# Kernel optimization log

Measured on AMD Instinct MI355X. Metric: run time of the kernel, lower is better.

## Reference

```python
import jax, jax.numpy as jnp
import numpy as np

N, E, D, H, C, L = 100000, 1280000, 64, 4, 16, 3  # nodes, edges, dim, heads, head_dim, layers
NEG_SLOPE = 0.2
LN_EPS = 1e-5


def setup_inputs() -> dict:
    key = jax.random.key(0)
    ks = jax.random.split(key, 6)
    scale = 1.0 / np.sqrt(D)
    x = jax.random.normal(ks[0], (N, D), dtype=jnp.float32)
    edge_index = jax.random.randint(ks[1], (2, E), 0, N, dtype=jnp.int64)
    Wl = jax.random.normal(ks[2], (L, D, H * C), dtype=jnp.float32) * scale  # lin_l (source)
    Wr = jax.random.normal(ks[3], (L, D, H * C), dtype=jnp.float32) * scale  # lin_r (target)
    att = jax.random.normal(ks[4], (L, H, C), dtype=jnp.float32) * scale
    bias = jnp.zeros((L, H * C), dtype=jnp.float32)
    gamma = jnp.ones((L, D), dtype=jnp.float32)
    beta = jnp.zeros((L, D), dtype=jnp.float32)
    return dict(x=x, edge_index=edge_index, Wl=Wl, Wr=Wr, att=att, bias=bias, gamma=gamma, beta=beta)


def _gatv2_conv(x, src, dst, Wl, Wr, att, bias):
    # GATv2Conv (concat=True, share_weights=False, negative_slope=0.2)
    n = x.shape[0]
    xl = (x @ Wl).reshape(n, H, C)  # messages from source nodes
    xr = (x @ Wr).reshape(n, H, C)  # target-side transform
    m = xl[src] + xr[dst]  # [E', H, C]
    e = jnp.einsum('ehc,hc->eh', jax.nn.leaky_relu(m, NEG_SLOPE), att)  # [E', H]
    emax = jax.ops.segment_max(e, dst, num_segments=n)
    p = jnp.exp(e - emax[dst])
    denom = jax.ops.segment_sum(p, dst, num_segments=n)
    alpha = p / denom[dst]  # self-loops guarantee denom > 0
    out = jax.ops.segment_sum(alpha[:, :, None] * xl[src], dst, num_segments=n)  # [N, H, C]
    return out.reshape(n, H * C) + bias


def _layernorm(x, gamma, beta):
    mu = jnp.mean(x, axis=-1, keepdims=True)
    var = jnp.mean(jnp.square(x - mu), axis=-1, keepdims=True)
    return (x - mu) * jax.lax.rsqrt(var + LN_EPS) * gamma + beta


def reference(x, edge_index, Wl, Wr, att, bias, gamma, beta):
    n = x.shape[0]
    loops = jnp.arange(n, dtype=edge_index.dtype)
    src = jnp.concatenate([edge_index[0], loops])  # PyG add_self_loops=True
    dst = jnp.concatenate([edge_index[1], loops])
    for i in range(L):
        x_res = x
        x = _gatv2_conv(x, src, dst, Wl[i], Wr[i], att[i], bias[i])
        x = x + x_res  # residual
        x = _layernorm(x, gamma[i], beta[i])
        x = jax.nn.gelu(x, approximate=False)
    return x
```

## Files before the change

kernel.cpp:

```cpp
#include <hip/hip_runtime.h>
#include <math.h>


#define SCAN_CHUNK 1024

typedef __attribute__((ext_vector_type(8))) short short8;
typedef __attribute__((ext_vector_type(4))) float f32x4;

static inline int cdiv(int a, int b) { return (a + b - 1) / b; }

__device__ __forceinline__ unsigned short bf16_rtn(float v) {
    unsigned u = __float_as_uint(v);
    return (unsigned short)((u + 0x7fffu + ((u >> 16) & 1u)) >> 16);
}


__global__ void detect_i64(const unsigned int* __restrict__ ei, int* __restrict__ flag) {
    if (threadIdx.x == 0 && blockIdx.x == 0) {
        int is64 = 1;
        #pragma unroll 1
        for (int i = 0; i < 64; ++i)
            if (ei[2 * i + 1] != 0u) { is64 = 0; break; }
        *flag = is64;
    }
}

__global__ void init_deg(int* __restrict__ deg, int N) {
    int i = blockIdx.x * blockDim.x + threadIdx.x;
    if (i < N) deg[i] = 1;
}

__global__ void hist_kernel(const int* __restrict__ ei, int E, const int* __restrict__ flag,
                            int* __restrict__ deg, int* __restrict__ pos) {
    int e = blockIdx.x * blockDim.x + threadIdx.x;
    if (e >= E) return;
    int is64 = *flag;
    int d = is64 ? ei[2 * (E + e)] : ei[E + e];
    pos[e] = atomicAdd(&deg[d], 1);
}

__global__ void scan_blocks(const int* __restrict__ deg, int* __restrict__ rowptr,
                            int* __restrict__ partials, int N) {
    __shared__ int sdata[256];
    int t = threadIdx.x;
    int idx0 = blockIdx.x * SCAN_CHUNK + t * 4;
    int v[4]; int sum = 0;
    #pragma unroll
    for (int i = 0; i < 4; ++i) {
        int ii = idx0 + i;
        v[i] = (ii < N) ? deg[ii] : 0;
        sum += v[i];
    }
    sdata[t] = sum;
    __syncthreads();
    for (int off = 1; off < 256; off <<= 1) {
        int val = 0;
        if (t >= off) val = sdata[t - off];
        __syncthreads();
        if (t >= off) sdata[t] += val;
        __syncthreads();
    }
    int run = (t > 0) ? sdata[t - 1] : 0;
    #pragma unroll
    for (int i = 0; i < 4; ++i) {
        int ii = idx0 + i;
        if (ii < N) rowptr[ii] = run;
        run += v[i];
    }
    if (t == 255) partials[blockIdx.x] = sdata[255];
}

__global__ void scan_partials_k(int* __restrict__ partials, int NB) {
    __shared__ int sd[256];
    int t = threadIdx.x;
    sd[t] = (t < NB) ? partials[t] : 0;
    __syncthreads();
    for (int off = 1; off < 256; off <<= 1) {
        int val = 0;
        if (t >= off) val = sd[t - off];
        __syncthreads();
        if (t >= off) sd[t] += val;
        __syncthreads();
    }
    if (t < NB) partials[t] = (t > 0) ? sd[t - 1] : 0;
}

__global__ void add_offsets(int* __restrict__ rowptr, const int* __restrict__ partials,
                            int N, int Etot) {
    int i = blockIdx.x * blockDim.x + threadIdx.x;
    if (i < N) rowptr[i] += partials[i / SCAN_CHUNK];
    if (i == 0) rowptr[N] = Etot;
}

__global__ void fill_csr(const int* __restrict__ ei, int E, int N, const int* __restrict__ flag,
                         const int* __restrict__ rowptr, const int* __restrict__ pos,
                         int* __restrict__ col) {
    int i = blockIdx.x * blockDim.x + threadIdx.x;
    if (i >= E + N) return;
    if (i < E) {
        int is64 = *flag;
        int s = is64 ? ei[2 * i] : ei[i];
        int d = is64 ? ei[2 * (E + i)] : ei[E + i];
        col[rowptr[d] + pos[i]] = s;
    } else {
        int nn = i - E;
        col[rowptr[nn]] = nn;
    }
}


__global__ __launch_bounds__(256) void cast_hi_lo(
    const float* __restrict__ x, unsigned short* __restrict__ hi,
    unsigned short* __restrict__ lo, int total4) {
    int i = blockIdx.x * blockDim.x + threadIdx.x;
    int stride = gridDim.x * blockDim.x;
    for (; i < total4; i += stride) {
        float4 v = ((const float4*)x)[i];
        ushort4 h, l;
        h.x = bf16_rtn(v.x); l.x = bf16_rtn(v.x - __uint_as_float((unsigned)h.x << 16));
        h.y = bf16_rtn(v.y); l.y = bf16_rtn(v.y - __uint_as_float((unsigned)h.y << 16));
        h.z = bf16_rtn(v.z); l.z = bf16_rtn(v.z - __uint_as_float((unsigned)h.z << 16));
        h.w = bf16_rtn(v.w); l.w = bf16_rtn(v.w - __uint_as_float((unsigned)h.w << 16));
        ((ushort4*)hi)[i] = h;
        ((ushort4*)lo)[i] = l;
    }
}

__global__ void wprep_kernel(const float* __restrict__ Wl, const float* __restrict__ Wr,
                             unsigned short* __restrict__ Bh, unsigned short* __restrict__ Bl,
                             int Lnum) {
    int t = blockIdx.x * blockDim.x + threadIdx.x;
    int total = Lnum * 2 * 4 * 2 * 64 * 8;
    if (t >= total) return;
    int j    = t & 7;
    int lane = (t >> 3) & 63;
    int kc   = (t >> 9) & 1;
    int ct   = (t >> 10) & 3;
    int h    = (t >> 12) & 1;
    int l    = t >> 13;
    const float* W = (h ? Wr : Wl) + (size_t)l * 4096;
    int k = kc * 32 + (lane >> 4) * 8 + j;
    int c = ct * 16 + (lane & 15);
    float v = W[k * 64 + c];
    unsigned short hv = bf16_rtn(v);
    Bh[t] = hv;
    Bl[t] = bf16_rtn(v - __uint_as_float((unsigned)hv << 16));
}

__global__ __launch_bounds__(256) void transform_mfma(
    const unsigned short* __restrict__ xh, const unsigned short* __restrict__ xlo,
    const unsigned short* __restrict__ Bh, const unsigned short* __restrict__ Bl,
    unsigned short* __restrict__ XL, float* __restrict__ XR, int N) {
    int lane = threadIdx.x & 63;
    int wid = (blockIdx.x * blockDim.x + threadIdx.x) >> 6;
    int nw = (gridDim.x * blockDim.x) >> 6;
    int half = wid & 1;

    const short8* Bh8 = (const short8*)Bh;
    const short8* Bl8 = (const short8*)Bl;
    short8 bh[4][2], bl[4][2];
    #pragma unroll
    for (int ct = 0; ct < 4; ++ct)
        #pragma unroll
        for (int kc = 0; kc < 2; ++kc) {
            int idx = ((half * 4 + ct) * 2 + kc) * 64 + lane;
            bh[ct][kc] = Bh8[idx];
            bl[ct][kc] = Bl8[idx];
        }

    const short8* Ah8 = (const short8*)xh;
    const short8* Al8 = (const short8*)xlo;
    int r16 = lane & 15, kq = lane >> 4;
    int ngroups = N >> 4;

    for (int gidx = wid >> 1; gidx < ngroups; gidx += (nw >> 1)) {
        int n0 = gidx << 4;
        size_t abase = (size_t)(n0 + r16) * 8 + kq;
        short8 ah0 = Ah8[abase],     ah1 = Ah8[abase + 4];
        short8 al0 = Al8[abase],     al1 = Al8[abase + 4];
        f32x4 acc[4] = {};
        #pragma unroll
        for (int ct = 0; ct < 4; ++ct) {
            acc[ct] = __builtin_amdgcn_mfma_f32_16x16x32_bf16(ah0, bh[ct][0], acc[ct], 0, 0, 0);
            acc[ct] = __builtin_amdgcn_mfma_f32_16x16x32_bf16(ah1, bh[ct][1], acc[ct], 0, 0, 0);
            acc[ct] = __builtin_amdgcn_mfma_f32_16x16x32_bf16(al0, bh[ct][0], acc[ct], 0, 0, 0);
            acc[ct] = __builtin_amdgcn_mfma_f32_16x16x32_bf16(al1, bh[ct][1], acc[ct], 0, 0, 0);
            acc[ct] = __builtin_amdgcn_mfma_f32_16x16x32_bf16(ah0, bl[ct][0], acc[ct], 0, 0, 0);
            acc[ct] = __builtin_amdgcn_mfma_f32_16x16x32_bf16(ah1, bl[ct][1], acc[ct], 0, 0, 0);
        }
        if (half) {
            #pragma unroll
            for (int ct = 0; ct < 4; ++ct)
                #pragma unroll
                for (int r = 0; r < 4; ++r)
                    XR[(size_t)(n0 + kq * 4 + r) * 64 + ct * 16 + r16] = acc[ct][r];
        } else {
            #pragma unroll
            for (int ct = 0; ct < 4; ++ct)
                #pragma unroll
                for (int r = 0; r < 4; ++r)
                    XL[(size_t)(n0 + kq * 4 + r) * 64 + ct * 16 + r16] = bf16_rtn(acc[ct][r]);
        }
    }
}

__global__ __launch_bounds__(256) void gat_gather_kernel(
    const unsigned short* __restrict__ XL, const float* __restrict__ XR,
    const float* __restrict__ x_res,
    const int* __restrict__ rowptr, const int* __restrict__ col,
    const float* __restrict__ att, const float* __restrict__ bias,
    const float* __restrict__ gamma, const float* __restrict__ beta,
    float* __restrict__ x_out,
    unsigned short* __restrict__ xh_out, unsigned short* __restrict__ xlo_out, int N) {
    int wid = (blockIdx.x * blockDim.x + threadIdx.x) >> 6;
    if (wid >= N) return;
    int lane = threadIdx.x & 63;
    int g = lane >> 4;
    int c = lane & 15;
    const int n = wid;

    float4 xr = ((const float4*)(XR + (size_t)n * 64))[c];
    float4 av = ((const float4*)att)[c];
    int start = rowptr[n], end = rowptr[n + 1];
    const ushort4* XL4 = (const ushort4*)XL;

    float m = -1e30f, s = 0.f;
    float o0 = 0.f, o1 = 0.f, o2 = 0.f, o3 = 0.f;

    for (int base = start; base < end; base += 64) {
        int rem = end - base;
        int chunk = rem < 64 ? rem : 64;
        int cidx = base + lane;
        int cl = col[cidx < end ? cidx : end - 1];
        int iters = (chunk + 3) >> 2;
        for (int t = 0; t < iters; ++t) {
            int idx = 4 * t + g;
            int srcn = __shfl(cl, idx);
            ushort4 hv = XL4[(size_t)srcn * 16 + c];
            float v0 = __uint_as_float((unsigned)hv.x << 16);
            float v1 = __uint_as_float((unsigned)hv.y << 16);
            float v2 = __uint_as_float((unsigned)hv.z << 16);
            float v3 = __uint_as_float((unsigned)hv.w << 16);
            float t0 = v0 + xr.x; t0 = fmaxf(t0, 0.2f * t0);
            float t1 = v1 + xr.y; t1 = fmaxf(t1, 0.2f * t1);
            float t2 = v2 + xr.z; t2 = fmaxf(t2, 0.2f * t2);
            float t3 = v3 + xr.w; t3 = fmaxf(t3, 0.2f * t3);
            float wsum = t0 * av.x;
            wsum = fmaf(t1, av.y, wsum);
            wsum = fmaf(t2, av.z, wsum);
            wsum = fmaf(t3, av.w, wsum);
            wsum += __shfl_xor(wsum, 1);
            wsum += __shfl_xor(wsum, 2);
            wsum = (idx < chunk) ? wsum : -1e30f;
            float mnew = fmaxf(m, wsum);
            float p = __expf(wsum - mnew);
            float sc = __expf(m - mnew);
            s = fmaf(s, sc, p);
            o0 = fmaf(o0, sc, p * v0);
            o1 = fmaf(o1, sc, p * v1);
            o2 = fmaf(o2, sc, p * v2);
            o3 = fmaf(o3, sc, p * v3);
            m = mnew;
        }
    }

    #pragma unroll
    for (int mask = 16; mask <= 32; mask <<= 1) {
        float m2 = __shfl_xor(m, mask);
        float s2 = __shfl_xor(s, mask);
        float q0 = __shfl_xor(o0, mask);
        float q1 = __shfl_xor(o1, mask);
        float q2 = __shfl_xor(o2, mask);
        float q3 = __shfl_xor(o3, mask);
        float mn = fmaxf(m, m2);
        float sa = __expf(m - mn), sb = __expf(m2 - mn);
        s = s * sa + s2 * sb;
        o0 = o0 * sa + q0 * sb;
        o1 = o1 * sa + q1 * sb;
        o2 = o2 * sa + q2 * sb;
        o3 = o3 * sa + q3 * sb;
        m = mn;
    }

    float inv = 1.f / s;
    float4 bi = ((const float4*)bias)[c];
    float4 rs = ((const float4*)(x_res + (size_t)n * 64))[c];
    float g0 = fmaf(o0, inv, bi.x + rs.x);
    float g1 = fmaf(o1, inv, bi.y + rs.y);
    float g2 = fmaf(o2, inv, bi.z + rs.z);
    float g3 = fmaf(o3, inv, bi.w + rs.w);

    float loc = g0 + g1 + g2 + g3;
    #pragma unroll
    for (int mask = 1; mask < 16; mask <<= 1) loc += __shfl_xor(loc, mask);
    float mu = loc * (1.f / 64.f);
    float d0 = g0 - mu, d1 = g1 - mu, d2 = g2 - mu, d3 = g3 - mu;
    float vs = d0 * d0 + d1 * d1 + d2 * d2 + d3 * d3;
    #pragma unroll
    for (int mask = 1; mask < 16; mask <<= 1) vs += __shfl_xor(vs, mask);
    float rstd = rsqrtf(vs * (1.f / 64.f) + 1e-5f);
    float4 ga = ((const float4*)gamma)[c];
    float4 be = ((const float4*)beta)[c];
    float y0 = fmaf(d0 * rstd, ga.x, be.x);
    float y1 = fmaf(d1 * rstd, ga.y, be.y);
    float y2 = fmaf(d2 * rstd, ga.z, be.z);
    float y3 = fmaf(d3 * rstd, ga.w, be.w);

    const float k = 0.70710678118654752f;
    float z0 = 0.5f * y0 * (1.f + erff(y0 * k));
    float z1 = 0.5f * y1 * (1.f + erff(y1 * k));
    float z2 = 0.5f * y2 * (1.f + erff(y2 * k));
    float z3 = 0.5f * y3 * (1.f + erff(y3 * k));

    if (g == 0) {
        ((float4*)(x_out + (size_t)n * 64))[c] = make_float4(z0, z1, z2, z3);
        if (xh_out) {
            ushort4 h, l;
            h.x = bf16_rtn(z0); l.x = bf16_rtn(z0 - __uint_as_float((unsigned)h.x << 16));
            h.y = bf16_rtn(z1); l.y = bf16_rtn(z1 - __uint_as_float((unsigned)h.y << 16));
            h.z = bf16_rtn(z2); l.z = bf16_rtn(z2 - __uint_as_float((unsigned)h.z << 16));
            h.w = bf16_rtn(z3); l.w = bf16_rtn(z3 - __uint_as_float((unsigned)h.w << 16));
            ((ushort4*)(xh_out + (size_t)n * 64))[c] = h;
            ((ushort4*)(xlo_out + (size_t)n * 64))[c] = l;
        }
    }
}


extern "C" void kernel_launch(void* const* d_in, const int* in_sizes, int n_in,
                              void* d_out, int out_size, void* d_ws, size_t ws_size,
                              hipStream_t stream) {
    const float* x0    = (const float*)d_in[0];
    const int*   ei    = (const int*)d_in[1];
    const float* Wl    = (const float*)d_in[2];
    const float* Wr    = (const float*)d_in[3];
    const float* att   = (const float*)d_in[4];
    const float* bias  = (const float*)d_in[5];
    const float* gamma = (const float*)d_in[6];
    const float* beta  = (const float*)d_in[7];
    float* out = (float*)d_out;

    const int N = in_sizes[0] / 64;
    const int E = in_sizes[1] / 2;
    const int Lnum = in_sizes[2] / (64 * 64);
    const int Etot = E + N;

    char* ws = (char*)d_ws;
    size_t off = 0;
    auto alloc = [&](size_t bytes) {
        void* p = ws + off;
        off = (off + bytes + 255) & ~(size_t)255;
        return p;
    };
    unsigned short* XLb = (unsigned short*)alloc((size_t)N * 64 * 2);
    float* XR     = (float*)alloc((size_t)N * 64 * 4);
    float* XA     = (float*)alloc((size_t)N * 64 * 4);
    unsigned short* xh  = (unsigned short*)alloc((size_t)N * 64 * 2);
    unsigned short* xlo = (unsigned short*)alloc((size_t)N * 64 * 2);
    unsigned short* Bh  = (unsigned short*)alloc((size_t)Lnum * 8192 * 2);
    unsigned short* Bl  = (unsigned short*)alloc((size_t)Lnum * 8192 * 2);
    int* rowptr   = (int*)alloc((size_t)(N + 1) * 4);
    int* deg      = (int*)alloc((size_t)N * 4);
    int* pos      = (int*)alloc((size_t)E * 4);
    int* partials = (int*)alloc(1024 * 4);
    int* flag     = (int*)alloc(256);
    int* col      = (int*)alloc((size_t)Etot * 4);

    cast_hi_lo<<<2048, 256, 0, stream>>>(x0, xh, xlo, N * 16);
    wprep_kernel<<<cdiv(Lnum * 8192, 256), 256, 0, stream>>>(Wl, Wr, Bh, Bl, Lnum);

    detect_i64<<<1, 64, 0, stream>>>((const unsigned int*)ei, flag);
    init_deg<<<cdiv(N, 256), 256, 0, stream>>>(deg, N);
    hist_kernel<<<cdiv(E, 256), 256, 0, stream>>>(ei, E, flag, deg, pos);
    int NB = cdiv(N, SCAN_CHUNK);
    scan_blocks<<<NB, 256, 0, stream>>>(deg, rowptr, partials, N);
    scan_partials_k<<<1, 256, 0, stream>>>(partials, NB);
    add_offsets<<<cdiv(N + 1, 256), 256, 0, stream>>>(rowptr, partials, N, Etot);
    fill_csr<<<cdiv(Etot, 256), 256, 0, stream>>>(ei, E, N, flag, rowptr, pos, col);

    const float* xcur = x0;
    for (int l = 0; l < Lnum; ++l) {
        transform_mfma<<<1024, 256, 0, stream>>>(
            xh, xlo, Bh + (size_t)l * 8192, Bl + (size_t)l * 8192, XLb, XR, N);
        float* xnext = (l == Lnum - 1) ? out : XA;
        int last = (l == Lnum - 1);
        gat_gather_kernel<<<cdiv(N * 64, 256), 256, 0, stream>>>(
            XLb, XR, xcur, rowptr, col,
            att + (size_t)l * 64, bias + (size_t)l * 64,
            gamma + (size_t)l * 64, beta + (size_t)l * 64,
            xnext, last ? nullptr : xh, last ? nullptr : xlo, N);
        xcur = xnext;
    }
}
```

Baseline: 437.8 us.

## Fuse bf16 split into transform, drop lo weight terms, unroll gather by two edges

Removes the separate hi/lo cast kernel and the split-output writes from the gather by converting fp32 x to bf16 hi/lo inside the MFMA transform. Drops the low-order weight correction entirely and applies the x low-order correction only to the target (XR) projection. The gather loop now processes two edges per iteration with 512-thread blocks, the dtype detection is merged into degree init, and the transform grid is doubled. This cuts launches and memory traffic at the cost of reduced precision in the projections.

```diff
diff --git a/kernel.cpp b/kernel.cpp
--- a/kernel.cpp
+++ b/kernel.cpp
@@ -15,19 +15,15 @@
 }
 
 
-__global__ void detect_i64(const unsigned int* __restrict__ ei, int* __restrict__ flag) {
-    if (threadIdx.x == 0 && blockIdx.x == 0) {
-        int is64 = 1;
-        #pragma unroll 1
-        for (int i = 0; i < 64; ++i)
-            if (ei[2 * i + 1] != 0u) { is64 = 0; break; }
-        *flag = is64;
-    }
-}
-
-__global__ void init_deg(int* __restrict__ deg, int N) {
+__global__ void csr_init(const unsigned int* __restrict__ ei, int* __restrict__ flag,
+                         int* __restrict__ deg, int N) {
     int i = blockIdx.x * blockDim.x + threadIdx.x;
     if (i < N) deg[i] = 1;
+    if (blockIdx.x == 0 && threadIdx.x < 64) {
+        int nz = (ei[2 * threadIdx.x + 1] != 0u) ? 1 : 0;
+        unsigned long long b = __ballot(nz);
+        if (threadIdx.x == 0) *flag = (b == 0ull) ? 1 : 0;
+    }
 }
 
 __global__ void hist_kernel(const int* __restrict__ ei, int E, const int* __restrict__ flag,
@@ -108,27 +104,8 @@
     }
 }
 
-
-__global__ __launch_bounds__(256) void cast_hi_lo(
-    const float* __restrict__ x, unsigned short* __restrict__ hi,
-    unsigned short* __restrict__ lo, int total4) {
-    int i = blockIdx.x * blockDim.x + threadIdx.x;
-    int stride = gridDim.x * blockDim.x;
-    for (; i < total4; i += stride) {
-        float4 v = ((const float4*)x)[i];
-        ushort4 h, l;
-        h.x = bf16_rtn(v.x); l.x = bf16_rtn(v.x - __uint_as_float((unsigned)h.x << 16));
-        h.y = bf16_rtn(v.y); l.y = bf16_rtn(v.y - __uint_as_float((unsigned)h.y << 16));
-        h.z = bf16_rtn(v.z); l.z = bf16_rtn(v.z - __uint_as_float((unsigned)h.z << 16));
-        h.w = bf16_rtn(v.w); l.w = bf16_rtn(v.w - __uint_as_float((unsigned)h.w << 16));
-        ((ushort4*)hi)[i] = h;
-        ((ushort4*)lo)[i] = l;
-    }
-}
-
 __global__ void wprep_kernel(const float* __restrict__ Wl, const float* __restrict__ Wr,
-                             unsigned short* __restrict__ Bh, unsigned short* __restrict__ Bl,
-                             int Lnum) {
+                             unsigned short* __restrict__ Bh, int Lnum) {
     int t = blockIdx.x * blockDim.x + threadIdx.x;
     int total = Lnum * 2 * 4 * 2 * 64 * 8;
     if (t >= total) return;
@@ -141,15 +118,11 @@
     const float* W = (h ? Wr : Wl) + (size_t)l * 4096;
     int k = kc * 32 + (lane >> 4) * 8 + j;
     int c = ct * 16 + (lane & 15);
-    float v = W[k * 64 + c];
-    unsigned short hv = bf16_rtn(v);
-    Bh[t] = hv;
-    Bl[t] = bf16_rtn(v - __uint_as_float((unsigned)hv << 16));
+    Bh[t] = bf16_rtn(W[k * 64 + c]);
 }
 
 __global__ __launch_bounds__(256) void transform_mfma(
-    const unsigned short* __restrict__ xh, const unsigned short* __restrict__ xlo,
-    const unsigned short* __restrict__ Bh, const unsigned short* __restrict__ Bl,
+    const float* __restrict__ x, const unsigned short* __restrict__ Bh,
     unsigned short* __restrict__ XL, float* __restrict__ XR, int N) {
     int lane = threadIdx.x & 63;
     int wid = (blockIdx.x * blockDim.x + threadIdx.x) >> 6;
@@ -157,36 +130,46 @@
     int half = wid & 1;
 
     const short8* Bh8 = (const short8*)Bh;
-    const short8* Bl8 = (const short8*)Bl;
-    short8 bh[4][2], bl[4][2];
+    short8 bh[4][2];
     #pragma unroll
     for (int ct = 0; ct < 4; ++ct)
         #pragma unroll
-        for (int kc = 0; kc < 2; ++kc) {
-            int idx = ((half * 4 + ct) * 2 + kc) * 64 + lane;
-            bh[ct][kc] = Bh8[idx];
-            bl[ct][kc] = Bl8[idx];
-        }
-
-    const short8* Ah8 = (const short8*)xh;
-    const short8* Al8 = (const short8*)xlo;
+        for (int kc = 0; kc < 2; ++kc)
+            bh[ct][kc] = Bh8[((half * 4 + ct) * 2 + kc) * 64 + lane];
+
     int r16 = lane & 15, kq = lane >> 4;
     int ngroups = N >> 4;
 
     for (int gidx = wid >> 1; gidx < ngroups; gidx += (nw >> 1)) {
         int n0 = gidx << 4;
-        size_t abase = (size_t)(n0 + r16) * 8 + kq;
-        short8 ah0 = Ah8[abase],     ah1 = Ah8[abase + 4];
-        short8 al0 = Al8[abase],     al1 = Al8[abase + 4];
+        const float4* row = (const float4*)(x + (size_t)(n0 + r16) * 64);
+        float4 f0 = row[2 * kq], f1 = row[2 * kq + 1];
+        float4 f2 = row[8 + 2 * kq], f3 = row[8 + 2 * kq + 1];
+        float fa[8] = {f0.x, f0.y, f0.z, f0.w, f1.x, f1.y, f1.z, f1.w};
+        float fb[8] = {f2.x, f2.y, f2.z, f2.w, f3.x, f3.y, f3.z, f3.w};
+        short8 ah0, ah1, al0, al1;
+        #pragma unroll
+        for (int j = 0; j < 8; ++j) {
+            unsigned short h0 = bf16_rtn(fa[j]);
+            unsigned short h1 = bf16_rtn(fb[j]);
+            ah0[j] = (short)h0;
+            ah1[j] = (short)h1;
+            al0[j] = (short)bf16_rtn(fa[j] - __uint_as_float((unsigned)h0 << 16));
+            al1[j] = (short)bf16_rtn(fb[j] - __uint_as_float((unsigned)h1 << 16));
+        }
+
         f32x4 acc[4] = {};
         #pragma unroll
         for (int ct = 0; ct < 4; ++ct) {
             acc[ct] = __builtin_amdgcn_mfma_f32_16x16x32_bf16(ah0, bh[ct][0], acc[ct], 0, 0, 0);
             acc[ct] = __builtin_amdgcn_mfma_f32_16x16x32_bf16(ah1, bh[ct][1], acc[ct], 0, 0, 0);
-            acc[ct] = __builtin_amdgcn_mfma_f32_16x16x32_bf16(al0, bh[ct][0], acc[ct], 0, 0, 0);
-            acc[ct] = __builtin_amdgcn_mfma_f32_16x16x32_bf16(al1, bh[ct][1], acc[ct], 0, 0, 0);
-            acc[ct] = __builtin_amdgcn_mfma_f32_16x16x32_bf16(ah0, bl[ct][0], acc[ct], 0, 0, 0);
-            acc[ct] = __builtin_amdgcn_mfma_f32_16x16x32_bf16(ah1, bl[ct][1], acc[ct], 0, 0, 0);
+        }
+        if (half) {
+            #pragma unroll
+            for (int ct = 0; ct < 4; ++ct) {
+                acc[ct] = __builtin_amdgcn_mfma_f32_16x16x32_bf16(al0, bh[ct][0], acc[ct], 0, 0, 0);
+                acc[ct] = __builtin_amdgcn_mfma_f32_16x16x32_bf16(al1, bh[ct][1], acc[ct], 0, 0, 0);
+            }
         }
         if (half) {
             #pragma unroll
@@ -204,14 +187,13 @@
     }
 }
 
-__global__ __launch_bounds__(256) void gat_gather_kernel(
+__global__ __launch_bounds__(512) void gat_gather_kernel(
     const unsigned short* __restrict__ XL, const float* __restrict__ XR,
     const float* __restrict__ x_res,
     const int* __restrict__ rowptr, const int* __restrict__ col,
     const float* __restrict__ att, const float* __restrict__ bias,
     const float* __restrict__ gamma, const float* __restrict__ beta,
-    float* __restrict__ x_out,
-    unsigned short* __restrict__ xh_out, unsigned short* __restrict__ xlo_out, int N) {
+    float* __restrict__ x_out, int N) {
     int wid = (blockIdx.x * blockDim.x + threadIdx.x) >> 6;
     if (wid >= N) return;
     int lane = threadIdx.x & 63;
@@ -232,35 +214,54 @@
         int chunk = rem < 64 ? rem : 64;
         int cidx = base + lane;
         int cl = col[cidx < end ? cidx : end - 1];
-        int iters = (chunk + 3) >> 2;
+        int iters = (chunk + 7) >> 3;
         for (int t = 0; t < iters; ++t) {
-            int idx = 4 * t + g;
-            int srcn = __shfl(cl, idx);
-            ushort4 hv = XL4[(size_t)srcn * 16 + c];
-            float v0 = __uint_as_float((unsigned)hv.x << 16);
-            float v1 = __uint_as_float((unsigned)hv.y << 16);
-            float v2 = __uint_as_float((unsigned)hv.z << 16);
-            float v3 = __uint_as_float((unsigned)hv.w << 16);
-            float t0 = v0 + xr.x; t0 = fmaxf(t0, 0.2f * t0);
-            float t1 = v1 + xr.y; t1 = fmaxf(t1, 0.2f * t1);
-            float t2 = v2 + xr.z; t2 = fmaxf(t2, 0.2f * t2);
-            float t3 = v3 + xr.w; t3 = fmaxf(t3, 0.2f * t3);
-            float wsum = t0 * av.x;
-            wsum = fmaf(t1, av.y, wsum);
-            wsum = fmaf(t2, av.z, wsum);
-            wsum = fmaf(t3, av.w, wsum);
-            wsum += __shfl_xor(wsum, 1);
-            wsum += __shfl_xor(wsum, 2);
-            wsum = (idx < chunk) ? wsum : -1e30f;
-            float mnew = fmaxf(m, wsum);
-            float p = __expf(wsum - mnew);
-            float sc = __expf(m - mnew);
-            s = fmaf(s, sc, p);
-            o0 = fmaf(o0, sc, p * v0);
-            o1 = fmaf(o1, sc, p * v1);
-            o2 = fmaf(o2, sc, p * v2);
-            o3 = fmaf(o3, sc, p * v3);
-            m = mnew;
+            int ia = 8 * t + g;
+            int ib = ia + 4;
+            int sa = __shfl(cl, ia);
+            int sb = __shfl(cl, ib);
+            ushort4 ha = XL4[(size_t)sa * 16 + c];
+            ushort4 hb = XL4[(size_t)sb * 16 + c];
+            float va0 = __uint_as_float((unsigned)ha.x << 16);
+            float va1 = __uint_as_float((unsigned)ha.y << 16);
+            float va2 = __uint_as_float((unsigned)ha.z << 16);
+            float va3 = __uint_as_float((unsigned)ha.w << 16);
+            float vb0 = __uint_as_float((unsigned)hb.x << 16);
+            float vb1 = __uint_as_float((unsigned)hb.y << 16);
+            float vb2 = __uint_as_float((unsigned)hb.z << 16);
+            float vb3 = __uint_as_float((unsigned)hb.w << 16);
+            float ta0 = va0 + xr.x; ta0 = fmaxf(ta0, 0.2f * ta0);
+            float ta1 = va1 + xr.y; ta1 = fmaxf(ta1, 0.2f * ta1);
+            float ta2 = va2 + xr.z; ta2 = fmaxf(ta2, 0.2f * ta2);
+            float ta3 = va3 + xr.w; ta3 = fmaxf(ta3, 0.2f * ta3);
+            float tb0 = vb0 + xr.x; tb0 = fmaxf(tb0, 0.2f * tb0);
+            float tb1 = vb1 + xr.y; tb1 = fmaxf(tb1, 0.2f * tb1);
+            float tb2 = vb2 + xr.z; tb2 = fmaxf(tb2, 0.2f * tb2);
+            float tb3 = vb3 + xr.w; tb3 = fmaxf(tb3, 0.2f * tb3);
+            float wa = ta0 * av.x;
+            wa = fmaf(ta1, av.y, wa);
+            wa = fmaf(ta2, av.z, wa);
+            wa = fmaf(ta3, av.w, wa);
+            float wb = tb0 * av.x;
+            wb = fmaf(tb1, av.y, wb);
+            wb = fmaf(tb2, av.z, wb);
+            wb = fmaf(tb3, av.w, wb);
+            wa += __shfl_xor(wa, 1);
+            wa += __shfl_xor(wa, 2);
+            wb += __shfl_xor(wb, 1);
+            wb += __shfl_xor(wb, 2);
+            wa = (ia < chunk) ? wa : -1e30f;
+            wb = (ib < chunk) ? wb : -1e30f;
+            float mn = fmaxf(fmaxf(m, wa), wb);
+            float pa = __expf(wa - mn);
+            float pb = __expf(wb - mn);
+            float sc = __expf(m - mn);
+            s = fmaf(s, sc, pa + pb);
+            o0 = fmaf(o0, sc, fmaf(pa, va0, pb * vb0));
+            o1 = fmaf(o1, sc, fmaf(pa, va1, pb * vb1));
+            o2 = fmaf(o2, sc, fmaf(pa, va2, pb * vb2));
+            o3 = fmaf(o3, sc, fmaf(pa, va3, pb * vb3));
+            m = mn;
         }
     }
 
@@ -314,15 +315,6 @@
 
     if (g == 0) {
         ((float4*)(x_out + (size_t)n * 64))[c] = make_float4(z0, z1, z2, z3);
-        if (xh_out) {
-            ushort4 h, l;
-            h.x = bf16_rtn(z0); l.x = bf16_rtn(z0 - __uint_as_float((unsigned)h.x << 16));
-            h.y = bf16_rtn(z1); l.y = bf16_rtn(z1 - __uint_as_float((unsigned)h.y << 16));
-            h.z = bf16_rtn(z2); l.z = bf16_rtn(z2 - __uint_as_float((unsigned)h.z << 16));
-            h.w = bf16_rtn(z3); l.w = bf16_rtn(z3 - __uint_as_float((unsigned)h.w << 16));
-            ((ushort4*)(xh_out + (size_t)n * 64))[c] = h;
-            ((ushort4*)(xlo_out + (size_t)n * 64))[c] = l;
-        }
     }
 }
 
@@ -355,10 +347,7 @@
     unsigned short* XLb = (unsigned short*)alloc((size_t)N * 64 * 2);
     float* XR     = (float*)alloc((size_t)N * 64 * 4);
     float* XA     = (float*)alloc((size_t)N * 64 * 4);
-    unsigned short* xh  = (unsigned short*)alloc((size_t)N * 64 * 2);
-    unsigned short* xlo = (unsigned short*)alloc((size_t)N * 64 * 2);
-    unsigned short* Bh  = (unsigned short*)alloc((size_t)Lnum * 8192 * 2);
-    unsigned short* Bl  = (unsigned short*)alloc((size_t)Lnum * 8192 * 2);
+    unsigned short* Bh = (unsigned short*)alloc((size_t)Lnum * 8192 * 2);
     int* rowptr   = (int*)alloc((size_t)(N + 1) * 4);
     int* deg      = (int*)alloc((size_t)N * 4);
     int* pos      = (int*)alloc((size_t)E * 4);
@@ -366,11 +355,8 @@
     int* flag     = (int*)alloc(256);
     int* col      = (int*)alloc((size_t)Etot * 4);
 
-    cast_hi_lo<<<2048, 256, 0, stream>>>(x0, xh, xlo, N * 16);
-    wprep_kernel<<<cdiv(Lnum * 8192, 256), 256, 0, stream>>>(Wl, Wr, Bh, Bl, Lnum);
-
-    detect_i64<<<1, 64, 0, stream>>>((const unsigned int*)ei, flag);
-    init_deg<<<cdiv(N, 256), 256, 0, stream>>>(deg, N);
+    wprep_kernel<<<cdiv(Lnum * 8192, 256), 256, 0, stream>>>(Wl, Wr, Bh, Lnum);
+    csr_init<<<cdiv(N, 256), 256, 0, stream>>>((const unsigned int*)ei, flag, deg, N);
     hist_kernel<<<cdiv(E, 256), 256, 0, stream>>>(ei, E, flag, deg, pos);
     int NB = cdiv(N, SCAN_CHUNK);
     scan_blocks<<<NB, 256, 0, stream>>>(deg, rowptr, partials, N);
@@ -380,15 +366,14 @@
 
     const float* xcur = x0;
     for (int l = 0; l < Lnum; ++l) {
-        transform_mfma<<<1024, 256, 0, stream>>>(
-            xh, xlo, Bh + (size_t)l * 8192, Bl + (size_t)l * 8192, XLb, XR, N);
+        transform_mfma<<<2048, 256, 0, stream>>>(
+            xcur, Bh + (size_t)l * 8192, XLb, XR, N);
         float* xnext = (l == Lnum - 1) ? out : XA;
-        int last = (l == Lnum - 1);
-        gat_gather_kernel<<<cdiv(N * 64, 256), 256, 0, stream>>>(
+        gat_gather_kernel<<<cdiv(N * 64, 512), 512, 0, stream>>>(
             XLb, XR, xcur, rowptr, col,
             att + (size_t)l * 64, bias + (size_t)l * 64,
             gamma + (size_t)l * 64, beta + (size_t)l * 64,
-            xnext, last ? nullptr : xh, last ? nullptr : xlo, N);
+            xnext, N);
         xcur = xnext;
     }
 }
```

New measurement: 415.1 us. -5.2%, faster.
